# Performance work log

Hardware: AMD Instinct MI355X
Metric: run time of the kernel (lower is better)

Reference implementation:

```python
import jax, jax.numpy as jnp
import numpy as np

K = 3
OFFSET_SCALE = 0.25
GN_GROUPS = 8
GN_EPS = 1e-5


def setup_inputs() -> dict:
    key = jax.random.key(0)
    k1, k2, k3 = jax.random.split(key, 3)
    N, C, H, W = 4, 128, 96, 96
    Cout = 128
    x = jax.random.normal(k1, (N, C, H, W), dtype=jnp.float32)
    # offset head: small random weights so offsets are modest (tanh tames anyway)
    w_head = jax.random.normal(k2, (3, C, 3, 3), dtype=jnp.float32) * 0.05
    b_head = jnp.zeros((3,), dtype=jnp.float32)
    # kaiming-ish scale for the deform conv weight: sqrt(2 / fan_out)
    w_dcn = jax.random.normal(k3, (Cout, C, 3, 3), dtype=jnp.float32) * np.sqrt(2.0 / (Cout * 9))
    gn_gamma = jnp.ones((Cout,), dtype=jnp.float32)
    gn_beta = jnp.zeros((Cout,), dtype=jnp.float32)
    return {"x": x, "w_head": w_head, "b_head": b_head, "w_dcn": w_dcn,
            "gn_gamma": gn_gamma, "gn_beta": gn_beta}


def _conv3x3(x, w, b):
    y = jax.lax.conv_general_dilated(
        x, w, window_strides=(1, 1), padding=((1, 1), (1, 1)),
        dimension_numbers=("NCHW", "OIHW", "NCHW"))
    return y + b[None, :, None, None]


def _deform_sample(xn, py, px):
    # xn: (C,H,W); py/px: (9,H,W) absolute sampling coords (y=row, x=col)
    C, H, W = xn.shape
    y0 = jnp.floor(py).astype(jnp.int32)
    x0 = jnp.floor(px).astype(jnp.int32)
    fy = py - y0
    fx = px - x0
    xf = xn.reshape(C, H * W)

    def corner(yi, xi, wgt):
        valid = (yi >= 0) & (yi < H) & (xi >= 0) & (xi < W)
        idx = jnp.clip(yi, 0, H - 1) * W + jnp.clip(xi, 0, W - 1)  # (9,H,W)
        v = xf[:, idx.reshape(-1)].reshape(C, *idx.shape)  # (C,9,H,W)
        return v * (wgt * valid)[None]

    return (corner(y0, x0, (1 - fy) * (1 - fx))
            + corner(y0, x0 + 1, (1 - fy) * fx)
            + corner(y0 + 1, x0, fy * (1 - fx))
            + corner(y0 + 1, x0 + 1, fy * fx))


def reference(x, w_head, b_head, w_dcn, gn_gamma, gn_beta):
    N, C, H, W = x.shape
    Cout = w_dcn.shape[0]
    stride, pad, dil = 1, 1, 1

    head = _conv3x3(x, w_head, b_head)                 # (N,3,H,W)
    dx, dy, m = head[:, :1], head[:, 1:2], head[:, 2:3]
    mask = jax.nn.sigmoid(m)                           # (N,1,H,W) broadcast over 9 taps
    dx = OFFSET_SCALE * jnp.tanh(dx)
    dy = OFFSET_SCALE * jnp.tanh(dy)

    # serpentine 18-channel offsets, mmcv layout: (oy, ox) pairs per kernel tap
    z = jnp.zeros_like(dx)
    offs = jnp.concatenate(
        [z, z, z, dy, z, -dy, dx, z, z, z, -dx, z, dx, dy, dx, -dy, -dx, dy], axis=1)
    offs = offs.reshape(N, 9, 2, H, W)
    oy, ox = offs[:, :, 0], offs[:, :, 1]              # (N,9,H,W)

    ky = jnp.arange(9) // 3
    kx = jnp.arange(9) % 3
    base_y = (jnp.arange(H) * stride - pad)[None, :, None] + (ky * dil)[:, None, None]
    base_x = (jnp.arange(W) * stride - pad)[None, None, :] + (kx * dil)[:, None, None]
    py = base_y[None] + oy                             # (N,9,H,W)
    px = base_x[None] + ox

    sampled = jax.vmap(_deform_sample)(x, py, px)      # (N,C,9,H,W)
    sampled = sampled * mask[:, None]                  # modulated

    y = jnp.einsum('nckhw,ock->nohw', sampled, w_dcn.reshape(Cout, C, 9))

    # GroupNorm(8, Cout) + ReLU
    G = min(GN_GROUPS, Cout)
    yg = y.reshape(N, G, Cout // G, H, W)
    mu = yg.mean(axis=(2, 3, 4), keepdims=True)
    var = yg.var(axis=(2, 3, 4), keepdims=True)
    yn = ((yg - mu) * jax.lax.rsqrt(var + GN_EPS)).reshape(N, Cout, H, W)
    yn = yn * gn_gamma[None, :, None, None] + gn_beta[None, :, None, None]
    return jax.nn.relu(yn)
```

## Files before the change

### kernel.cpp

```cpp
#include <hip/hip_runtime.h>
#include <hip/hip_bf16.h>
#include <math.h>

#define NB   4
#define CIN  128
#define HH   96
#define WW   96
#define HWN  (HH*WW)
#define NHW  (NB*HWN)
#define COUT 128
#define KW   9
#define KDIM (CIN*KW)
#define GSZ  16
#define PXB  32
#define NBLK (NHW/PXB)
#define XPB  64
#define XPOB (NHW/XPB)

typedef __attribute__((ext_vector_type(8))) short bf16x8;
typedef __attribute__((ext_vector_type(4))) float f32x4;

#define OFF_WAH   0
#define OFF_DX    147456
#define OFF_DY    184320
#define OFF_MASK  221184
#define OFF_GN    258048
#define OFF_MAP   258240
#define OFF_PAIR  258496
#define OFF_XT    258560

#define HEADB 1152

__device__ __forceinline__ ushort f2bf(float f) {
    union { float f; uint u; } v; v.f = f;
    uint r = v.u + 0x7fffu + ((v.u >> 16) & 1u);
    return (ushort)(r >> 16);
}

__device__ __forceinline__ void barrier_keep_vm() {
    asm volatile("s_waitcnt lgkmcnt(0)\n\ts_barrier" ::: "memory");
}

__global__ __launch_bounds__(256) void pre_kernel(const float* __restrict__ x,
                                                  const float* __restrict__ w_head,
                                                  const float* __restrict__ b_head,
                                                  const float* __restrict__ wd,
                                                  ushort* __restrict__ wah,
                                                  float* __restrict__ dxv,
                                                  float* __restrict__ dyv,
                                                  float* __restrict__ maskv,
                                                  float* __restrict__ gn_part,
                                                  int* __restrict__ map,
                                                  int* __restrict__ pairB,
                                                  float* __restrict__ xt) {
    __shared__ __attribute__((aligned(16))) float smem[8480];
    const int b = blockIdx.x, t = threadIdx.x;

    if (b >= HEADB + 576) {
        float (*tile)[XPB + 1] = (float (*)[XPB + 1])smem;
        int* sperm = (int*)(smem + CIN * (XPB + 1));
        int* spair = (int*)(smem + CIN * (XPB + 1) + CIN);
        const int bb2 = b - (HEADB + 576);
        const int p0 = bb2 * XPB;
        const int n  = p0 / HWN, hw0 = p0 % HWN;
        const float* xn = x + (size_t)n * CIN * HWN + hw0;

        if (t < 64) {
            int l = t;
            union { bf16x8 v; short a[8]; } B;
#pragma unroll
            for (int e = 0; e < 8; ++e) {
                float val = (float)(1u << (((l >> 4) * 8 + e) & 31));
                B.a[e] = (short)f2bf(val);
            }
#pragma unroll
            for (int s = 0; s < 32; ++s) {
                union { bf16x8 v; short a[8]; } A;
#pragma unroll
                for (int e = 0; e < 8; ++e) A.a[e] = 0;
                if ((l >> 4) == (s >> 3)) A.a[s & 7] = (short)f2bf(1.0f);
                f32x4 d = {0.f, 0.f, 0.f, 0.f};
                d = __builtin_amdgcn_mfma_f32_16x16x32_bf16(A.v, B.v, d, 0, 0, 0);
                float v0 = d[0];
                if (l == 0 && v0 > 0.f) {
                    int ex; frexpf(v0, &ex);
                    int j = ex - 1;
                    if (j >= 0 && j < 32) spair[j] = s;
                }
            }
        }
        __syncthreads();
        if (t < CIN) sperm[t] = (t & ~31) | (spair[t & 31] & 31);
        __syncthreads();

#pragma unroll
        for (int rep = 0; rep < 4; ++rep) {
            const int c  = rep * 32 + (t >> 3);
            const int px = (t & 7) * 8;
            const float* src = xn + (size_t)c * HWN + px;
            float4 a = *(const float4*)src;
            float4 bq = *(const float4*)(src + 4);
            tile[c][px + 0] = a.x;  tile[c][px + 1] = a.y;
            tile[c][px + 2] = a.z;  tile[c][px + 3] = a.w;
            tile[c][px + 4] = bq.x; tile[c][px + 5] = bq.y;
            tile[c][px + 6] = bq.z; tile[c][px + 7] = bq.w;
        }
        __syncthreads();

#pragma unroll
        for (int wc = 0; wc < 8; ++wc) {
            const int idx = wc * 256 + t;
            const int px  = idx >> 5;
            const int s4  = idx & 31;
            float4 v;
            v.x = tile[sperm[s4 * 4 + 0]][px];
            v.y = tile[sperm[s4 * 4 + 1]][px];
            v.z = tile[sperm[s4 * 4 + 2]][px];
            v.w = tile[sperm[s4 * 4 + 3]][px];
            *(float4*)(xt + ((size_t)(p0 + px)) * CIN + s4 * 4) = v;
        }
        return;
    }

    if (b >= HEADB) {
        const int bb = b - HEADB;
        int i = bb * 256 + t;
        {
            int e  = i & 7;
            int l  = (i >> 3) & 63;
            int ot = (i >> 9) & 7;
            int q  = (i >> 12) & 3;
            int k  = i >> 14;
            int o  = ot * 16 + (l & 15);
            int c  = q * 32 + (l >> 4) * 8 + e;
            wah[i] = f2bf(wd[o * KDIM + c * KW + k]);
        }
        if (bb == 0 && t < 128) gn_part[t] = 0.f;
        if (bb == 0 && t < 64) {
            int l = t;
            bf16x8 A1 = {}, B1 = {}, A2 = {}, B2 = {};
            if ((l >> 4) == 0) {
                A1[0] = (short)f2bf((float)((l & 15) + 1));
                B1[0] = (short)f2bf(1.0f);
                A2[0] = (short)f2bf(1.0f);
                B2[0] = (short)f2bf((float)((l & 15) + 1));
            }
            f32x4 d1 = {0.f,0.f,0.f,0.f}, d2 = {0.f,0.f,0.f,0.f};
            d1 = __builtin_amdgcn_mfma_f32_16x16x32_bf16(A1, B1, d1, 0, 0, 0);
            d2 = __builtin_amdgcn_mfma_f32_16x16x32_bf16(A2, B2, d2, 0, 0, 0);
#pragma unroll
            for (int r = 0; r < 4; ++r) {
                int m = (int)(d1[r] + 0.5f) - 1;
                int n = (int)(d2[r] + 0.5f) - 1;
                map[l * 4 + r] = (m << 4) | n;
            }
        }
        if (bb == 1 && t < 64) {
            int l = t;
            union { bf16x8 v; short a[8]; } B;
#pragma unroll
            for (int e = 0; e < 8; ++e) {
                float val = (float)(1u << (((l >> 4) * 8 + e) & 31));
                B.a[e] = (short)f2bf(val);
            }
#pragma unroll
            for (int s = 0; s < 32; ++s) {
                union { bf16x8 v; short a[8]; } A;
#pragma unroll
                for (int e = 0; e < 8; ++e) A.a[e] = 0;
                if ((l >> 4) == (s >> 3)) A.a[s & 7] = (short)f2bf(1.0f);
                f32x4 d = {0.f, 0.f, 0.f, 0.f};
                d = __builtin_amdgcn_mfma_f32_16x16x32_bf16(A.v, B.v, d, 0, 0, 0);
                float v0 = d[0];
                if (l == 0 && v0 > 0.f) {
                    int ex; frexpf(v0, &ex);
                    int j = ex - 1;
                    if (j >= 0 && j < 32) pairB[j] = s;
                }
            }
        }
        return;
    }

    float* wl = smem;
    float (*sp)[8][13] = (float (*)[8][13])(smem + CIN * 28);
    for (int i = t; i < 3456; i += 256) {
        int j = i / KDIM, r = i - j * KDIM;
        int c = r / 9, kk = r - c * 9;
        wl[c * 28 + kk * 3 + j] = w_head[i];
    }
    __syncthreads();

    const int sl = t & 7;
    const int cg = t >> 3;
    const int p0 = b * 32 + sl * 4;
    const int n  = p0 / HWN;
    const int hw = p0 - n * HWN;
    const int h  = hw / WW;
    const int w0 = hw - h * WW;
    const float* xn = x + (size_t)n * CIN * HWN;
    const bool lok = (w0 > 0);
    const bool rok = (w0 < WW - 4);

    float acc[12];
#pragma unroll
    for (int i = 0; i < 12; ++i) acc[i] = 0.f;

#pragma unroll
    for (int cc = 0; cc < 4; ++cc) {
        const int c = cg * 4 + cc;
        const float* xc = xn + (size_t)c * HWN;
        float v[3][6];
#pragma unroll
        for (int r = 0; r < 3; ++r) {
            int y = h - 1 + r;
            if (y >= 0 && y < HH) {
                const float* xr = xc + y * WW + w0;
                float4 m4 = *(const float4*)xr;
                v[r][1] = m4.x; v[r][2] = m4.y; v[r][3] = m4.z; v[r][4] = m4.w;
                v[r][0] = lok ? xr[-1] : 0.f;
                v[r][5] = rok ? xr[4]  : 0.f;
            } else {
#pragma unroll
                for (int i = 0; i < 6; ++i) v[r][i] = 0.f;
            }
        }
        float wr[28];
        const float* wc = &wl[c * 28];
#pragma unroll
        for (int i2 = 0; i2 < 7; ++i2) {
            float4 q4 = *(const float4*)(wc + i2 * 4);
            wr[i2 * 4 + 0] = q4.x; wr[i2 * 4 + 1] = q4.y;
            wr[i2 * 4 + 2] = q4.z; wr[i2 * 4 + 3] = q4.w;
        }
#pragma unroll
        for (int ky = 0; ky < 3; ++ky)
#pragma unroll
            for (int kx = 0; kx < 3; ++kx) {
                const int kk = ky * 3 + kx;
                const float wj0 = wr[kk * 3 + 0];
                const float wj1 = wr[kk * 3 + 1];
                const float wj2 = wr[kk * 3 + 2];
#pragma unroll
                for (int q = 0; q < 4; ++q) {
                    float val = v[ky][q + kx];
                    acc[q * 3 + 0] = fmaf(val, wj0, acc[q * 3 + 0]);
                    acc[q * 3 + 1] = fmaf(val, wj1, acc[q * 3 + 1]);
                    acc[q * 3 + 2] = fmaf(val, wj2, acc[q * 3 + 2]);
                }
            }
    }
#pragma unroll
    for (int i = 0; i < 12; ++i) sp[cg][sl][i] = acc[i];
    __syncthreads();
    if (cg < 8) {
#pragma unroll
        for (int k = 8; k < 32; k += 8)
#pragma unroll
            for (int i = 0; i < 12; ++i) sp[cg][sl][i] += sp[cg + k][sl][i];
    }
    __syncthreads();
    if (t < 32) {
        const int s2 = t >> 2, q = t & 3;
        float b0 = b_head[0], b1 = b_head[1], b2 = b_head[2];
#pragma unroll
        for (int cgi = 0; cgi < 8; ++cgi) {
            b0 += sp[cgi][s2][q * 3 + 0];
            b1 += sp[cgi][s2][q * 3 + 1];
            b2 += sp[cgi][s2][q * 3 + 2];
        }
        int pp = b * 32 + t;
        dxv[pp]   = 0.25f * tanhf(b0);
        dyv[pp]   = 0.25f * tanhf(b1);
        maskv[pp] = 1.f / (1.f + expf(-b2));
    }
}

__global__ __launch_bounds__(256, 3) void dcn_kernel(const float* __restrict__ xt,
                                                  const ushort* __restrict__ wah,
                                                  const float* __restrict__ dxv,
                                                  const float* __restrict__ dyv,
                                                  const float* __restrict__ maskv,
                                                  const int* __restrict__ map,
                                                  float* __restrict__ out,
                                                  float* __restrict__ gn_part) {
    __shared__ __attribute__((aligned(16))) ushort sBh[2][4 * PXB * 8];
    __shared__ float sMask[PXB];
    __shared__ float gred[16];

    const int t = threadIdx.x;
    const int lane = t & 63;
    const int wv = t >> 6;
    const int lg = lane >> 4;
    const int ml = lane & 15;
    const int pix = t >> 3;
    const int sg  = t & 7;

    int b = blockIdx.x;
    int nb = (b & 7) * (NBLK / 8) + (b >> 3);
    const int p0  = nb * PXB;
    const int n   = p0 / HWN;
    const int hw0 = p0 % HWN;
    const float* xtn = xt + (size_t)n * HWN * CIN;

    if (t < PXB) sMask[t] = maskv[p0 + t];
    if (t < 16) gred[t] = 0.f;

    const float dxl = dxv[p0 + pix];
    const float dyl = dyv[p0 + pix];
    const int hme = (hw0 + pix) / WW;
    const int wme = (hw0 + pix) % WW;

    f32x4 acc[2][2];
#pragma unroll
    for (int i = 0; i < 2; i++)
#pragma unroll
        for (int j = 0; j < 2; j++) acc[i][j] = (f32x4){0.f, 0.f, 0.f, 0.f};

    const int oyc[9] = {0, 0, 0, 1, 0, -1, 1, 1, -1};
    const int oxc[9] = {0, 1, -1, 0, 0, 0, 1, -1, 1};
    const int ncl[9] = {1, 2, 2, 2, 1, 2, 4, 4, 4};

    int    aa[2][4];
    float  wq[2][4];
    float4 vr[2][4];
    bf16x8 An[2][2];

#define CORNERS(kn_, cs_) {                                                    \
    const int ky = (kn_) / 3, kx = (kn_) - ky * 3;                             \
    float py = (float)(hme - 1 + ky) + (float)oyc[kn_] * dxl;                  \
    float px = (float)(wme - 1 + kx) + (float)oxc[kn_] * dyl;                  \
    float fy0 = floorf(py), fx0 = floorf(px);                                  \
    int y0 = (int)fy0, x0 = (int)fx0;                                          \
    float fy = py - fy0, fx = px - fx0;                                        \
    _Pragma("unroll")                                                          \
    for (int jj = 0; jj < 4; ++jj) {                                           \
        int yy = y0 + (jj >> 1), xx = x0 + (jj & 1);                           \
        float wb = ((jj >> 1) ? fy : 1.f - fy) * ((jj & 1) ? fx : 1.f - fx);   \
        bool ok = (yy >= 0) && (yy < HH) && (xx >= 0) && (xx < WW);            \
        aa[cs_][jj] = min(max(yy, 0), HH - 1) * WW + min(max(xx, 0), WW - 1);  \
        wq[cs_][jj] = ok ? wb : 0.f;                                           \
    }                                                                          \
    if (ncl[kn_] == 2 && oxc[kn_] == 0) {                                      \
        aa[cs_][1] = aa[cs_][2]; wq[cs_][1] = wq[cs_][2];                      \
    } }

#define ISSUE(jn_, rs_, cs_) {                                                 \
    const int qn_ = (jn_) & 3, NCn_ = ncl[(jn_) >> 2];                         \
    const int co_ = qn_ * 32 + sg * 4;                                         \
    vr[rs_][0] = *(const float4*)(xtn + ((aa[cs_][0] << 7) + co_));            \
    if (NCn_ >= 2) vr[rs_][1] = *(const float4*)(xtn + ((aa[cs_][1] << 7) + co_)); \
    if (NCn_ == 4) {                                                           \
        vr[rs_][2] = *(const float4*)(xtn + ((aa[cs_][2] << 7) + co_));        \
        vr[rs_][3] = *(const float4*)(xtn + ((aa[cs_][3] << 7) + co_));        \
    }                                                                          \
    const size_t abase_ = (size_t)((jn_) * 8 + wv * 2) * 512 + lane * 8;       \
    An[rs_][0] = *(const bf16x8*)(wah + abase_);                               \
    An[rs_][1] = *(const bf16x8*)(wah + abase_ + 512);                         \
    }

    CORNERS(0, 0);
    ISSUE(0, 0, 0);
    ISSUE(1, 1, 0);

#pragma unroll
    for (int j = 0; j < 36; ++j) {
        const int k  = j >> 2;
        const int NC = ncl[k];
        const int cs = k & 1;
        const int rs = j & 1;
        bf16x8 Ah0 = An[rs][0], Ah1 = An[rs][1];
        union { short4 v; ushort u[4]; } hv;
        {
            float s0 = vr[rs][0].x * wq[cs][0], s1 = vr[rs][0].y * wq[cs][0];
            float s2 = vr[rs][0].z * wq[cs][0], s3 = vr[rs][0].w * wq[cs][0];
            if (NC >= 2) {
                s0 = fmaf(vr[rs][1].x, wq[cs][1], s0); s1 = fmaf(vr[rs][1].y, wq[cs][1], s1);
                s2 = fmaf(vr[rs][1].z, wq[cs][1], s2); s3 = fmaf(vr[rs][1].w, wq[cs][1], s3);
            }
            if (NC == 4) {
                s0 = fmaf(vr[rs][2].x, wq[cs][2], s0); s1 = fmaf(vr[rs][2].y, wq[cs][2], s1);
                s2 = fmaf(vr[rs][2].z, wq[cs][2], s2); s3 = fmaf(vr[rs][2].w, wq[cs][2], s3);
                s0 = fmaf(vr[rs][3].x, wq[cs][3], s0); s1 = fmaf(vr[rs][3].y, wq[cs][3], s1);
                s2 = fmaf(vr[rs][3].z, wq[cs][3], s2); s3 = fmaf(vr[rs][3].w, wq[cs][3], s3);
            }
            hv.u[0] = f2bf(s0); hv.u[1] = f2bf(s1);
            hv.u[2] = f2bf(s2); hv.u[3] = f2bf(s3);
        }
        const int wbase = ((sg >> 1) * PXB + pix) * 8 + (sg & 1) * 4;
        *(short4*)&sBh[rs][wbase] = hv.v;
        if (j < 34) {
            const int jn = j + 2, kn = jn >> 2, qn = jn & 3, csn = kn & 1;
            if (qn == 0) CORNERS(kn, csn);
            ISSUE(jn, rs, csn);
        }
        barrier_keep_vm();
#pragma unroll
        for (int pt = 0; pt < 2; ++pt) {
            const int rbase = (lg * PXB + pt * 16 + ml) * 8;
            bf16x8 Bh = *(const bf16x8*)&sBh[rs][rbase];
            acc[0][pt] = __builtin_amdgcn_mfma_f32_16x16x32_bf16(Ah0, Bh, acc[0][pt], 0, 0, 0);
            acc[1][pt] = __builtin_amdgcn_mfma_f32_16x16x32_bf16(Ah1, Bh, acc[1][pt], 0, 0, 0);
        }
    }
#undef CORNERS
#undef ISSUE

    int4 mn4 = *(const int4*)&map[lane * 4];
    int mn[4] = {mn4.x, mn4.y, mn4.z, mn4.w};
    float s1g[2] = {0.f, 0.f}, s2g[2] = {0.f, 0.f};
#pragma unroll
    for (int ot = 0; ot < 2; ++ot) {
        int otile = wv * 32 + ot * 16;
#pragma unroll
        for (int pt = 0; pt < 2; ++pt) {
#pragma unroll
            for (int r = 0; r < 4; ++r) {
                int m = mn[r] >> 4, nn2 = mn[r] & 15;
                int p = pt * 16 + nn2;
                float v = acc[ot][pt][r] * sMask[p];
                s1g[ot] += v;
                s2g[ot] += v * v;
                out[((size_t)n * COUT + otile + m) * HWN + hw0 + p] = v;
            }
        }
    }
#pragma unroll
    for (int ot = 0; ot < 2; ++ot) {
        int g = wv * 2 + ot;
        atomicAdd(&gred[g * 2 + 0], s1g[ot]);
        atomicAdd(&gred[g * 2 + 1], s2g[ot]);
    }
    __syncthreads();
    if (t < 8) {
        atomicAdd(&gn_part[n * 8 + t],      gred[t * 2 + 0]);
        atomicAdd(&gn_part[64 + n * 8 + t], gred[t * 2 + 1]);
    }
}

__global__ __launch_bounds__(256) void gn_apply(float* __restrict__ out,
                                                const float* __restrict__ gn_part,
                                                const float* __restrict__ gamma,
                                                const float* __restrict__ beta) {
    int i4 = blockIdx.x * 256 + threadIdx.x;
    size_t e = (size_t)i4 * 4;
    int og = (int)(e / HWN);
    int n = og >> 7, o = og & 127;
    int s = n * 8 + (o >> 4);
    const float cnt = (float)GSZ * (float)HWN;
    float s1 = gn_part[s], s2 = gn_part[64 + s];
    float mu = s1 / cnt;
    float var = s2 / cnt - mu * mu;
    float inv = rsqrtf(var + 1e-5f);
    float ga = gamma[o] * inv;
    float be = beta[o] - mu * ga;
    float4 v = *(float4*)(out + e);
    v.x = fmaxf(fmaf(v.x, ga, be), 0.f);
    v.y = fmaxf(fmaf(v.y, ga, be), 0.f);
    v.z = fmaxf(fmaf(v.z, ga, be), 0.f);
    v.w = fmaxf(fmaf(v.w, ga, be), 0.f);
    *(float4*)(out + e) = v;
}

extern "C" void kernel_launch(void* const* d_in, const int* in_sizes, int n_in,
                              void* d_out, int out_size, void* d_ws, size_t ws_size,
                              hipStream_t stream) {
    const float* x       = (const float*)d_in[0];
    const float* w_head  = (const float*)d_in[1];
    const float* b_head  = (const float*)d_in[2];
    const float* w_dcn   = (const float*)d_in[3];
    const float* gamma   = (const float*)d_in[4];
    const float* beta    = (const float*)d_in[5];
    float* out = (float*)d_out;
    float* ws  = (float*)d_ws;

    ushort* wah    = (ushort*)(ws + OFF_WAH);
    float* dxv     = ws + OFF_DX;
    float* dyv     = ws + OFF_DY;
    float* maskv   = ws + OFF_MASK;
    float* gn_part = ws + OFF_GN;
    int*   map     = (int*)(ws + OFF_MAP);
    int*   pairB   = (int*)(ws + OFF_PAIR);
    float* xt      = ws + OFF_XT;

    pre_kernel<<<HEADB + 576 + XPOB, 256, 0, stream>>>(x, w_head, b_head, w_dcn, wah,
                                                       dxv, dyv, maskv, gn_part, map, pairB, xt);
    dcn_kernel<<<NBLK, 256, 0, stream>>>(xt, wah, dxv, dyv, maskv, map, out, gn_part);
    gn_apply<<<(NB * COUT * HWN) / 4 / 256, 256, 0, stream>>>(out, gn_part, gamma, beta);
}
```

Before: 157.9 us.

## Stage all 36 sampled B tiles in LDS and run MFMAs after one barrier

Replaces the per-step double-buffered LDS exchange, which needed a barrier on each of the 36 K-steps, with a full 36-slice LDS buffer. The gather and bilinear phase writes every slice first, then a single __syncthreads precedes a separate MFMA loop that software-pipelines the A (weight) and B (LDS) loads. This removes 35 barriers and decouples gather latency from MFMA issue. In exchange LDS use per block grows to about 72KB, the launch-bounds occupancy hint drops from 3 to 2 blocks, and the gather and MFMA work no longer overlap within a block.

```diff
diff --git a/kernel.cpp b/kernel.cpp
--- a/kernel.cpp
+++ b/kernel.cpp
@@ -37,10 +37,6 @@
     return (ushort)(r >> 16);
 }
 
-__device__ __forceinline__ void barrier_keep_vm() {
-    asm volatile("s_waitcnt lgkmcnt(0)\n\ts_barrier" ::: "memory");
-}
-
 __global__ __launch_bounds__(256) void pre_kernel(const float* __restrict__ x,
                                                   const float* __restrict__ w_head,
                                                   const float* __restrict__ b_head,
@@ -276,7 +272,7 @@
     }
 }
 
-__global__ __launch_bounds__(256, 3) void dcn_kernel(const float* __restrict__ xt,
+__global__ __launch_bounds__(256, 2) void dcn_kernel(const float* __restrict__ xt,
                                                   const ushort* __restrict__ wah,
                                                   const float* __restrict__ dxv,
                                                   const float* __restrict__ dyv,
@@ -284,7 +280,7 @@
                                                   const int* __restrict__ map,
                                                   float* __restrict__ out,
                                                   float* __restrict__ gn_part) {
-    __shared__ __attribute__((aligned(16))) ushort sBh[2][4 * PXB * 8];
+    __shared__ __attribute__((aligned(16))) ushort sB[36][4 * PXB * 8];
     __shared__ float sMask[PXB];
     __shared__ float gred[16];
 
@@ -324,7 +320,6 @@
     int    aa[2][4];
     float  wq[2][4];
     float4 vr[2][4];
-    bf16x8 An[2][2];
 
 #define CORNERS(kn_, cs_) {                                                    \
     const int ky = (kn_) / 3, kx = (kn_) - ky * 3;                             \
@@ -353,23 +348,19 @@
     if (NCn_ == 4) {                                                           \
         vr[rs_][2] = *(const float4*)(xtn + ((aa[cs_][2] << 7) + co_));        \
         vr[rs_][3] = *(const float4*)(xtn + ((aa[cs_][3] << 7) + co_));        \
-    }                                                                          \
-    const size_t abase_ = (size_t)((jn_) * 8 + wv * 2) * 512 + lane * 8;       \
-    An[rs_][0] = *(const bf16x8*)(wah + abase_);                               \
-    An[rs_][1] = *(const bf16x8*)(wah + abase_ + 512);                         \
-    }
+    } }
 
     CORNERS(0, 0);
     ISSUE(0, 0, 0);
     ISSUE(1, 1, 0);
 
+    const int wbase = ((sg >> 1) * PXB + pix) * 8 + (sg & 1) * 4;
 #pragma unroll
     for (int j = 0; j < 36; ++j) {
         const int k  = j >> 2;
         const int NC = ncl[k];
         const int cs = k & 1;
         const int rs = j & 1;
-        bf16x8 Ah0 = An[rs][0], Ah1 = An[rs][1];
         union { short4 v; ushort u[4]; } hv;
         {
             float s0 = vr[rs][0].x * wq[cs][0], s1 = vr[rs][0].y * wq[cs][0];
@@ -387,24 +378,44 @@
             hv.u[0] = f2bf(s0); hv.u[1] = f2bf(s1);
             hv.u[2] = f2bf(s2); hv.u[3] = f2bf(s3);
         }
-        const int wbase = ((sg >> 1) * PXB + pix) * 8 + (sg & 1) * 4;
-        *(short4*)&sBh[rs][wbase] = hv.v;
+        *(short4*)&sB[j][wbase] = hv.v;
         if (j < 34) {
             const int jn = j + 2, kn = jn >> 2, qn = jn & 3, csn = kn & 1;
             if (qn == 0) CORNERS(kn, csn);
             ISSUE(jn, rs, csn);
         }
-        barrier_keep_vm();
-#pragma unroll
-        for (int pt = 0; pt < 2; ++pt) {
-            const int rbase = (lg * PXB + pt * 16 + ml) * 8;
-            bf16x8 Bh = *(const bf16x8*)&sBh[rs][rbase];
-            acc[0][pt] = __builtin_amdgcn_mfma_f32_16x16x32_bf16(Ah0, Bh, acc[0][pt], 0, 0, 0);
-            acc[1][pt] = __builtin_amdgcn_mfma_f32_16x16x32_bf16(Ah1, Bh, acc[1][pt], 0, 0, 0);
-        }
     }
 #undef CORNERS
 #undef ISSUE
+
+    __syncthreads();
+
+    const int rbase0 = (lg * PXB + ml) * 8;
+    const int rbase1 = (lg * PXB + 16 + ml) * 8;
+    bf16x8 Ac0, Ac1, Bc0, Bc1;
+    {
+        const size_t ab = (size_t)(wv * 2) * 512 + lane * 8;
+        Ac0 = *(const bf16x8*)(wah + ab);
+        Ac1 = *(const bf16x8*)(wah + ab + 512);
+        Bc0 = *(const bf16x8*)&sB[0][rbase0];
+        Bc1 = *(const bf16x8*)&sB[0][rbase1];
+    }
+#pragma unroll
+    for (int j = 0; j < 36; ++j) {
+        bf16x8 An0, An1, Bn0, Bn1;
+        if (j < 35) {
+            const size_t ab = (size_t)((j + 1) * 8 + wv * 2) * 512 + lane * 8;
+            An0 = *(const bf16x8*)(wah + ab);
+            An1 = *(const bf16x8*)(wah + ab + 512);
+            Bn0 = *(const bf16x8*)&sB[j + 1][rbase0];
+            Bn1 = *(const bf16x8*)&sB[j + 1][rbase1];
+        }
+        acc[0][0] = __builtin_amdgcn_mfma_f32_16x16x32_bf16(Ac0, Bc0, acc[0][0], 0, 0, 0);
+        acc[1][0] = __builtin_amdgcn_mfma_f32_16x16x32_bf16(Ac1, Bc0, acc[1][0], 0, 0, 0);
+        acc[0][1] = __builtin_amdgcn_mfma_f32_16x16x32_bf16(Ac0, Bc1, acc[0][1], 0, 0, 0);
+        acc[1][1] = __builtin_amdgcn_mfma_f32_16x16x32_bf16(Ac1, Bc1, acc[1][1], 0, 0, 0);
+        if (j < 35) { Ac0 = An0; Ac1 = An1; Bc0 = Bn0; Bc1 = Bn1; }
+    }
 
     int4 mn4 = *(const int4*)&map[lane * 4];
     int mn[4] = {mn4.x, mn4.y, mn4.z, mn4.w};
```

Result: slower. 162.6 us (+3.0%).
